# Optimization experiments

Hardware: AMD Instinct MI355X
Metric: run time of the kernel (lower is better)

Reference implementation:

```python
import jax, jax.numpy as jnp
import numpy as np

NI = 2048           # per-node feature dim
H = 2 * NI          # flattened per-sample GRU state (2 nodes)
BS = 4096
NO = 1
NUM_ROUNDS = 2


def setup_inputs() -> dict:
    key = jax.random.key(0)
    ks = jax.random.split(key, 8)
    s_ih = 1.0 / np.sqrt(H)
    features = jax.random.normal(ks[0], (BS, 2, NI), dtype=jnp.float32)
    # torch.nn.GRUCell(H, H): weight_ih [3H, H], weight_hh [3H, H], biases [3H]
    W_ih = jax.random.uniform(ks[1], (3 * H, H), minval=-s_ih, maxval=s_ih, dtype=jnp.float32)
    b_ih = jax.random.uniform(ks[2], (3 * H,), minval=-s_ih, maxval=s_ih, dtype=jnp.float32)
    W_hh = jax.random.uniform(ks[3], (3 * H, H), minval=-s_ih, maxval=s_ih, dtype=jnp.float32)
    b_hh = jax.random.uniform(ks[4], (3 * H,), minval=-s_ih, maxval=s_ih, dtype=jnp.float32)
    # fc = nn.Linear(2*ni, no)
    fc_w = jax.random.uniform(ks[5], (NO, H), minval=-s_ih, maxval=s_ih, dtype=jnp.float32)
    fc_b = jax.random.uniform(ks[6], (NO,), minval=-s_ih, maxval=s_ih, dtype=jnp.float32)
    return {"features": features, "W_ih": W_ih, "b_ih": b_ih,
            "W_hh": W_hh, "b_hh": b_hh, "fc_w": fc_w, "fc_b": fc_b}


def _gru_cell(x, h, W_ih, b_ih, W_hh, b_hh):
    # torch GRUCell semantics
    gi = x @ W_ih.T + b_ih              # [bs, 3H]
    gh = h @ W_hh.T + b_hh              # [bs, 3H]
    i_r, i_z, i_n = jnp.split(gi, 3, axis=-1)
    h_r, h_z, h_n = jnp.split(gh, 3, axis=-1)
    r = jax.nn.sigmoid(i_r + h_r)
    z = jax.nn.sigmoid(i_z + h_z)
    n = jnp.tanh(i_n + r * h_n)
    return (1.0 - z) * n + z * h


def reference(features, W_ih, b_ih, W_hh, b_hh, fc_w, fc_b):
    bs = features.shape[0]
    ni = features.shape[2]
    h = features.reshape(bs, -1)        # [bs, 2*ni] = node0 || node1
    for _ in range(NUM_ROUNDS):
        # fully-connected 2-node graph, sum-aggregate of neighbor messages:
        # node0 receives h1, node1 receives h0 -> x is the half-swap of h
        x = jnp.concatenate([h[:, ni:], h[:, :ni]], axis=-1)
        h = _gru_cell(x, h, W_ih, b_ih, W_hh, b_hh)
    return h @ fc_w.T + fc_b            # [bs, no]
```

## Files before the change

kernel.cpp:

```cpp
#include <hip/hip_runtime.h>


typedef __bf16 bf16x8 __attribute__((ext_vector_type(8)));
typedef float  f32x4  __attribute__((ext_vector_type(4)));
typedef unsigned short u16x4 __attribute__((ext_vector_type(4)));

#define HH    4096
#define NI_D  2048
#define N3H   12288
#define N6H   24576
#define BSZ   4096
#define BM    256
#define BN    256
#define BK    64
#define MT    (BSZ / BM)
#define NT    (N6H / BN)
#define GRID_GEMM (MT * NT)
#define NKT   (HH / BK)

#define NB_W  98304
#define NB_C  16384

__device__ __forceinline__ unsigned short f2bf(float f) {
  unsigned u = __float_as_uint(f);
  u += 0x7FFFu + ((u >> 16) & 1u);
  return (unsigned short)(u >> 16);
}
__device__ __forceinline__ float bf2f(unsigned short s) {
  return __uint_as_float(((unsigned)s) << 16);
}

__device__ __forceinline__ void gload16(const void* g, void* l) {
  void* gv = (void*)g;
  __builtin_amdgcn_global_load_lds(
      (__attribute__((address_space(1))) unsigned int*)gv,
      (__attribute__((address_space(3))) unsigned int*)l,
      16, 0, 0);
}

__global__ void __launch_bounds__(256)
prep(const float* __restrict__ Wih, const float* __restrict__ Whh,
     const float* __restrict__ feat,
     unsigned short* __restrict__ Wc, unsigned short* __restrict__ hb)
{
  int bid = blockIdx.x;
  if (bid < NB_W) {
    int idx = (bid * 256 + threadIdx.x) << 2;
    int j = idx >> 12;
    int k = idx & 4095;
    const float* src;
    if (j < N3H) src = Wih + (size_t)j * HH + ((k + NI_D) & (HH - 1));
    else         src = Whh + (size_t)(j - N3H) * HH + k;
    f32x4 v = *(const f32x4*)src;
    u16x4 o = { f2bf(v[0]), f2bf(v[1]), f2bf(v[2]), f2bf(v[3]) };
    *(u16x4*)(Wc + idx) = o;
  } else {
    int i = ((bid - NB_W) * 256 + threadIdx.x) << 2;
    f32x4 v = *(const f32x4*)(feat + i);
    u16x4 o = { f2bf(v[0]), f2bf(v[1]), f2bf(v[2]), f2bf(v[3]) };
    *(u16x4*)(hb + i) = o;
  }
}

__device__ __forceinline__ void stageA(const char* a_base, char* lds, int ldst,
                                       int d, int kt, int g) {
  int kc = (kt < NKT) ? kt : 0;
  gload16(a_base + (size_t)kc * 128 + (size_t)g * 524288,
          lds + d * 32768 + g * 8192 + ldst);
}
__device__ __forceinline__ void stageB(const char* b_base, char* lds, int ldst,
                                       int d, int kt, int g) {
  int kc = (kt < NKT) ? kt : 0;
  gload16(b_base + (size_t)kc * 128 + (size_t)g * 524288,
          lds + 65536 + d * 32768 + g * 8192 + ldst);
}

template <int MB, int NB>
__device__ __forceinline__ void mfmaQ(f32x4 (&acc)[8][4],
                                      const bf16x8 (&af)[4][2],
                                      const bf16x8 (&bf)[2][2]) {
  __builtin_amdgcn_s_setprio(1);
#pragma unroll
  for (int ks = 0; ks < 2; ++ks)
#pragma unroll
    for (int mf = 0; mf < 4; ++mf)
#pragma unroll
      for (int nf = 0; nf < 2; ++nf)
        acc[MB + mf][NB + nf] = __builtin_amdgcn_mfma_f32_16x16x32_bf16(
            af[mf][ks], bf[nf][ks], acc[MB + mf][NB + nf], 0, 0, 0);
  __builtin_amdgcn_s_setprio(0);
}

#define BAR   __builtin_amdgcn_s_barrier()
#define SB    __builtin_amdgcn_sched_barrier(0)
#define LGKM0 do { asm volatile("s_waitcnt lgkmcnt(0)" ::: "memory"); SB; } while (0)
#define VM6   asm volatile("s_waitcnt vmcnt(6)" ::: "memory")

template <int D>
__device__ __forceinline__ void kblock(char* lds, const char* a_base,
                                       const char* b_base, int ldst,
                                       int aro, int bro, int offk0, int offk1,
                                       int t1, int t2, f32x4 (&acc)[8][4],
                                       bf16x8 (&a47c)[4][2], bf16x8 (&b01c)[2][2],
                                       bf16x8 (&a47n)[4][2], bf16x8 (&b01n)[2][2]) {
  const char* LA  = lds + D * 32768 + aro;
  const char* LB  = lds + 65536 + D * 32768 + bro;
  const char* LAn = lds + (D ^ 1) * 32768 + aro;
  const char* LBn = lds + 65536 + (D ^ 1) * 32768 + bro;
  bf16x8 a03[4][2], b23[2][2];

  LGKM0;
#pragma unroll
  for (int nf = 0; nf < 2; ++nf) {
    b23[nf][0] = *(const bf16x8*)(LB + (2 + nf) * 2048 + offk0);
    b23[nf][1] = *(const bf16x8*)(LB + (2 + nf) * 2048 + offk1);
  }
  stageA(a_base, lds, ldst, D ^ 1, t1, 0);
  stageA(a_base, lds, ldst, D ^ 1, t1, 2);
  SB;
  mfmaQ<4, 0>(acc, a47c, b01c);
  VM6;
  BAR;

  LGKM0;
#pragma unroll
  for (int mf = 0; mf < 4; ++mf) {
    a03[mf][0] = *(const bf16x8*)(LA + mf * 2048 + offk0);
    a03[mf][1] = *(const bf16x8*)(LA + mf * 2048 + offk1);
  }
  stageA(a_base, lds, ldst, D, t2, 1);
  stageA(a_base, lds, ldst, D, t2, 3);
  SB;
  mfmaQ<4, 2>(acc, a47c, b23);
  BAR;

  LGKM0;
  stageB(b_base, lds, ldst, D, t2, 0);
  stageB(b_base, lds, ldst, D, t2, 1);
  SB;
  mfmaQ<0, 0>(acc, a03, b01c);
  VM6;
  BAR;

#pragma unroll
  for (int mf = 0; mf < 4; ++mf) {
    a47n[mf][0] = *(const bf16x8*)(LAn + (4 + mf) * 2048 + offk0);
    a47n[mf][1] = *(const bf16x8*)(LAn + (4 + mf) * 2048 + offk1);
  }
#pragma unroll
  for (int nf = 0; nf < 2; ++nf) {
    b01n[nf][0] = *(const bf16x8*)(LBn + nf * 2048 + offk0);
    b01n[nf][1] = *(const bf16x8*)(LBn + nf * 2048 + offk1);
  }
  stageB(b_base, lds, ldst, D, t2, 2);
  stageB(b_base, lds, ldst, D, t2, 3);
  SB;
  mfmaQ<0, 2>(acc, a03, b23);
  BAR;
}

__global__ void __launch_bounds__(512, 2)
gemm_bt(const unsigned short* __restrict__ A,
        const unsigned short* __restrict__ B,
        unsigned short* __restrict__ C)
{
  __shared__ alignas(16) char lds[131072];

  int bid = blockIdx.x;
  int wg  = (bid & 7) * (GRID_GEMM / 8) + (bid >> 3);
  int nt  = wg / MT;
  int mt  = wg % MT;
  int m0  = mt * BM;
  int n0  = nt * BN;

  int t  = threadIdx.x;
  int wv = t >> 6;
  int l  = t & 63;
  int wm = wv >> 2;
  int wn = wv & 3;

  int rloc   = wv * 8 + (l >> 3);
  int sg_col = ((l & 7) ^ (l >> 3)) << 4;
  const char* a_base = (const char*)A + (size_t)(m0 + rloc) * 8192 + sg_col;
  const char* b_base = (const char*)B + (size_t)(n0 + rloc) * 8192 + sg_col;
  int ldst = wv * 1024;

  int offk0 = ((l >> 4) << 4) ^ ((l & 7) << 4);
  int offk1 = offk0 ^ 64;
  int aro = (wm * 128 + (l & 15)) * 128;
  int bro = (wn * 64  + (l & 15)) * 128;

  f32x4 acc[8][4] = {};
  bf16x8 a47A[4][2], b01A[2][2], a47B[4][2], b01B[2][2];

#pragma unroll
  for (int g = 0; g < 4; ++g) stageA(a_base, lds, ldst, 0, 0, g);
#pragma unroll
  for (int g = 0; g < 4; ++g) stageB(b_base, lds, ldst, 0, 0, g);
  stageA(a_base, lds, ldst, 1, 1, 1);
  stageA(a_base, lds, ldst, 1, 1, 3);
#pragma unroll
  for (int g = 0; g < 4; ++g) stageB(b_base, lds, ldst, 1, 1, g);
  asm volatile("s_waitcnt vmcnt(6)" ::: "memory");
  BAR;
  {
    const char* LA0 = lds + aro;
    const char* LB0 = lds + 65536 + bro;
#pragma unroll
    for (int mf = 0; mf < 4; ++mf) {
      a47A[mf][0] = *(const bf16x8*)(LA0 + (4 + mf) * 2048 + offk0);
      a47A[mf][1] = *(const bf16x8*)(LA0 + (4 + mf) * 2048 + offk1);
    }
#pragma unroll
    for (int nf = 0; nf < 2; ++nf) {
      b01A[nf][0] = *(const bf16x8*)(LB0 + nf * 2048 + offk0);
      b01A[nf][1] = *(const bf16x8*)(LB0 + nf * 2048 + offk1);
    }
  }

#pragma unroll 1
  for (int tt = 0; tt < NKT; tt += 2) {
    kblock<0>(lds, a_base, b_base, ldst, aro, bro, offk0, offk1,
              tt + 1, tt + 2, acc, a47A, b01A, a47B, b01B);
    kblock<1>(lds, a_base, b_base, ldst, aro, bro, offk0, offk1,
              tt + 2, tt + 3, acc, a47B, b01B, a47A, b01A);
  }
  asm volatile("s_waitcnt vmcnt(0) lgkmcnt(0)" ::: "memory");

  int crow = m0 + wm * 128 + ((l >> 4) << 2);
  int ccol = n0 + wn * 64 + (l & 15);
#pragma unroll
  for (int mf = 0; mf < 8; ++mf)
#pragma unroll
    for (int nf = 0; nf < 4; ++nf)
#pragma unroll
      for (int i = 0; i < 4; ++i)
        C[(size_t)(crow + mf * 16 + i) * N6H + (ccol + nf * 16)] =
            f2bf(acc[mf][nf][i]);
}

__global__ void __launch_bounds__(256)
gru1(const unsigned short* __restrict__ C, const float* __restrict__ h_old,
     const float* __restrict__ b_ih, const float* __restrict__ b_hh,
     unsigned short* __restrict__ h_bf)
{
  int idx = blockIdx.x * 256 + threadIdx.x;
  int b = idx >> 10;
  int j = (idx & 1023) << 2;
  const unsigned short* Cr = C + (size_t)b * N6H;
  u16x4 gir = *(const u16x4*)(Cr + j);
  u16x4 giz = *(const u16x4*)(Cr + HH + j);
  u16x4 gin = *(const u16x4*)(Cr + 2 * HH + j);
  u16x4 ghr = *(const u16x4*)(Cr + 3 * HH + j);
  u16x4 ghz = *(const u16x4*)(Cr + 4 * HH + j);
  u16x4 ghn = *(const u16x4*)(Cr + 5 * HH + j);
  f32x4 bir = *(const f32x4*)(b_ih + j);
  f32x4 biz = *(const f32x4*)(b_ih + HH + j);
  f32x4 bin = *(const f32x4*)(b_ih + 2 * HH + j);
  f32x4 bhr = *(const f32x4*)(b_hh + j);
  f32x4 bhz = *(const f32x4*)(b_hh + HH + j);
  f32x4 bhn = *(const f32x4*)(b_hh + 2 * HH + j);
  f32x4 ho  = *(const f32x4*)(h_old + (size_t)b * HH + j);
  u16x4 hb;
#pragma unroll
  for (int e = 0; e < 4; ++e) {
    float r = 1.f / (1.f + expf(-(bf2f(gir[e]) + bir[e] + bf2f(ghr[e]) + bhr[e])));
    float z = 1.f / (1.f + expf(-(bf2f(giz[e]) + biz[e] + bf2f(ghz[e]) + bhz[e])));
    float n = tanhf(bf2f(gin[e]) + bin[e] + r * (bf2f(ghn[e]) + bhn[e]));
    hb[e] = f2bf((1.f - z) * n + z * ho[e]);
  }
  *(u16x4*)(h_bf + (size_t)b * HH + j) = hb;
}

__global__ void __launch_bounds__(256)
gru2_fc(const unsigned short* __restrict__ C,
        const unsigned short* __restrict__ h_old_bf,
        const float* __restrict__ b_ih, const float* __restrict__ b_hh,
        const float* __restrict__ fcw, const float* __restrict__ fcb,
        float* __restrict__ out)
{
  int idx = blockIdx.x * 256 + threadIdx.x;
  int b = idx >> 10;
  int j = (idx & 1023) << 2;
  const unsigned short* Cr = C + (size_t)b * N6H;
  u16x4 gir = *(const u16x4*)(Cr + j);
  u16x4 giz = *(const u16x4*)(Cr + HH + j);
  u16x4 gin = *(const u16x4*)(Cr + 2 * HH + j);
  u16x4 ghr = *(const u16x4*)(Cr + 3 * HH + j);
  u16x4 ghz = *(const u16x4*)(Cr + 4 * HH + j);
  u16x4 ghn = *(const u16x4*)(Cr + 5 * HH + j);
  f32x4 bir = *(const f32x4*)(b_ih + j);
  f32x4 biz = *(const f32x4*)(b_ih + HH + j);
  f32x4 bin = *(const f32x4*)(b_ih + 2 * HH + j);
  f32x4 bhr = *(const f32x4*)(b_hh + j);
  f32x4 bhz = *(const f32x4*)(b_hh + HH + j);
  f32x4 bhn = *(const f32x4*)(b_hh + 2 * HH + j);
  u16x4 hob = *(const u16x4*)(h_old_bf + (size_t)b * HH + j);
  f32x4 fw  = *(const f32x4*)(fcw + j);
  float s = 0.f;
#pragma unroll
  for (int e = 0; e < 4; ++e) {
    float r = 1.f / (1.f + expf(-(bf2f(gir[e]) + bir[e] + bf2f(ghr[e]) + bhr[e])));
    float z = 1.f / (1.f + expf(-(bf2f(giz[e]) + biz[e] + bf2f(ghz[e]) + bhz[e])));
    float n = tanhf(bf2f(gin[e]) + bin[e] + r * (bf2f(ghn[e]) + bhn[e]));
    float h = (1.f - z) * n + z * bf2f(hob[e]);
    s += h * fw[e];
  }
#pragma unroll
  for (int off = 32; off > 0; off >>= 1) s += __shfl_down(s, off);
  __shared__ float red[4];
  if ((threadIdx.x & 63) == 0) red[threadIdx.x >> 6] = s;
  __syncthreads();
  if (threadIdx.x == 0) {
    float v = red[0] + red[1] + red[2] + red[3];
    if ((blockIdx.x & 3) == 0) v += fcb[0];
    atomicAdd(&out[b], v);
  }
}

extern "C" void kernel_launch(void* const* d_in, const int* in_sizes, int n_in,
                              void* d_out, int out_size, void* d_ws, size_t ws_size,
                              hipStream_t stream)
{
  const float* feat = (const float*)d_in[0];
  const float* Wih  = (const float*)d_in[1];
  const float* bih  = (const float*)d_in[2];
  const float* Whh  = (const float*)d_in[3];
  const float* bhh  = (const float*)d_in[4];
  const float* fcw  = (const float*)d_in[5];
  const float* fcb  = (const float*)d_in[6];
  float* out = (float*)d_out;

  char* ws = (char*)d_ws;
  unsigned short* Wc   = (unsigned short*)ws;
  unsigned short* Cbuf = (unsigned short*)(ws + 201326592);
  unsigned short* hb   = (unsigned short*)(ws + 402653184);

  hipMemsetAsync(out, 0, (size_t)out_size * sizeof(float), stream);
  prep<<<NB_W + NB_C, 256, 0, stream>>>(Wih, Whh, feat, Wc, hb);

  gemm_bt<<<GRID_GEMM, 512, 0, stream>>>(hb, Wc, Cbuf);
  gru1<<<16384, 256, 0, stream>>>(Cbuf, feat, bih, bhh, hb);

  gemm_bt<<<GRID_GEMM, 512, 0, stream>>>(hb, Wc, Cbuf);
  gru2_fc<<<16384, 256, 0, stream>>>(Cbuf, hb, bih, bhh, fcw, fcb, out);
}
```

Baseline: 1.503 ms.

## Triple-buffer B tiles in LDS to prefetch weights further ahead

Adds a third LDS buffer for the B (weight) operand so B tiles are loaded three k-steps ahead while A stays double-buffered. The main loop is unrolled by six with rotating buffer indices, a fixed tail, and adjusted vmcnt waits. The intent is to hide more global-load latency behind MFMA work. The cost is larger LDS use, which may limit occupancy, and more code size.

```diff
diff --git a/kernel.cpp b/kernel.cpp
--- a/kernel.cpp
+++ b/kernel.cpp
@@ -69,10 +69,10 @@
           lds + d * 32768 + g * 8192 + ldst);
 }
 __device__ __forceinline__ void stageB(const char* b_base, char* lds, int ldst,
-                                       int d, int kt, int g) {
+                                       int q, int kt, int g) {
   int kc = (kt < NKT) ? kt : 0;
   gload16(b_base + (size_t)kc * 128 + (size_t)g * 524288,
-          lds + 65536 + d * 32768 + g * 8192 + ldst);
+          lds + 65536 + q * 32768 + g * 8192 + ldst);
 }
 
 template <int MB, int NB>
@@ -94,19 +94,21 @@
 #define BAR   __builtin_amdgcn_s_barrier()
 #define SB    __builtin_amdgcn_sched_barrier(0)
 #define LGKM0 do { asm volatile("s_waitcnt lgkmcnt(0)" ::: "memory"); SB; } while (0)
-#define VM6   asm volatile("s_waitcnt vmcnt(6)" ::: "memory")
-
-template <int D>
+#define VM8   asm volatile("s_waitcnt vmcnt(8)" ::: "memory")
+#define VM10  asm volatile("s_waitcnt vmcnt(10)" ::: "memory")
+
+template <int AD, int BD, int BD1>
 __device__ __forceinline__ void kblock(char* lds, const char* a_base,
                                        const char* b_base, int ldst,
                                        int aro, int bro, int offk0, int offk1,
-                                       int t1, int t2, f32x4 (&acc)[8][4],
+                                       int tA1, int tA2, int tB3,
+                                       f32x4 (&acc)[8][4],
                                        bf16x8 (&a47c)[4][2], bf16x8 (&b01c)[2][2],
                                        bf16x8 (&a47n)[4][2], bf16x8 (&b01n)[2][2]) {
-  const char* LA  = lds + D * 32768 + aro;
-  const char* LB  = lds + 65536 + D * 32768 + bro;
-  const char* LAn = lds + (D ^ 1) * 32768 + aro;
-  const char* LBn = lds + 65536 + (D ^ 1) * 32768 + bro;
+  const char* LA  = lds + AD * 32768 + aro;
+  const char* LB  = lds + 65536 + BD * 32768 + bro;
+  const char* LAn = lds + (AD ^ 1) * 32768 + aro;
+  const char* LBn = lds + 65536 + BD1 * 32768 + bro;
   bf16x8 a03[4][2], b23[2][2];
 
   LGKM0;
@@ -115,11 +117,11 @@
     b23[nf][0] = *(const bf16x8*)(LB + (2 + nf) * 2048 + offk0);
     b23[nf][1] = *(const bf16x8*)(LB + (2 + nf) * 2048 + offk1);
   }
-  stageA(a_base, lds, ldst, D ^ 1, t1, 0);
-  stageA(a_base, lds, ldst, D ^ 1, t1, 2);
+  stageA(a_base, lds, ldst, AD ^ 1, tA1, 0);
+  stageA(a_base, lds, ldst, AD ^ 1, tA1, 2);
   SB;
   mfmaQ<4, 0>(acc, a47c, b01c);
-  VM6;
+  VM8;
   BAR;
 
   LGKM0;
@@ -128,18 +130,18 @@
     a03[mf][0] = *(const bf16x8*)(LA + mf * 2048 + offk0);
     a03[mf][1] = *(const bf16x8*)(LA + mf * 2048 + offk1);
   }
-  stageA(a_base, lds, ldst, D, t2, 1);
-  stageA(a_base, lds, ldst, D, t2, 3);
+  stageA(a_base, lds, ldst, AD, tA2, 1);
+  stageA(a_base, lds, ldst, AD, tA2, 3);
   SB;
   mfmaQ<4, 2>(acc, a47c, b23);
   BAR;
 
   LGKM0;
-  stageB(b_base, lds, ldst, D, t2, 0);
-  stageB(b_base, lds, ldst, D, t2, 1);
+  stageB(b_base, lds, ldst, BD, tB3, 0);
+  stageB(b_base, lds, ldst, BD, tB3, 1);
   SB;
   mfmaQ<0, 0>(acc, a03, b01c);
-  VM6;
+  VM10;
   BAR;
 
 #pragma unroll
@@ -152,8 +154,8 @@
     b01n[nf][0] = *(const bf16x8*)(LBn + nf * 2048 + offk0);
     b01n[nf][1] = *(const bf16x8*)(LBn + nf * 2048 + offk1);
   }
-  stageB(b_base, lds, ldst, D, t2, 2);
-  stageB(b_base, lds, ldst, D, t2, 3);
+  stageB(b_base, lds, ldst, BD, tB3, 2);
+  stageB(b_base, lds, ldst, BD, tB3, 3);
   SB;
   mfmaQ<0, 2>(acc, a03, b23);
   BAR;
@@ -164,7 +166,7 @@
         const unsigned short* __restrict__ B,
         unsigned short* __restrict__ C)
 {
-  __shared__ alignas(16) char lds[131072];
+  __shared__ alignas(16) char lds[163840];
 
   int bid = blockIdx.x;
   int wg  = (bid & 7) * (GRID_GEMM / 8) + (bid >> 3);
@@ -194,14 +196,18 @@
   bf16x8 a47A[4][2], b01A[2][2], a47B[4][2], b01B[2][2];
 
 #pragma unroll
-  for (int g = 0; g < 4; ++g) stageA(a_base, lds, ldst, 0, 0, g);
-#pragma unroll
   for (int g = 0; g < 4; ++g) stageB(b_base, lds, ldst, 0, 0, g);
+  stageA(a_base, lds, ldst, 0, 0, 1);
+  stageA(a_base, lds, ldst, 0, 0, 3);
+#pragma unroll
+  for (int g = 0; g < 4; ++g) stageB(b_base, lds, ldst, 1, 1, g);
+  stageA(a_base, lds, ldst, 0, 0, 0);
+  stageA(a_base, lds, ldst, 0, 0, 2);
   stageA(a_base, lds, ldst, 1, 1, 1);
   stageA(a_base, lds, ldst, 1, 1, 3);
 #pragma unroll
-  for (int g = 0; g < 4; ++g) stageB(b_base, lds, ldst, 1, 1, g);
-  asm volatile("s_waitcnt vmcnt(6)" ::: "memory");
+  for (int g = 0; g < 4; ++g) stageB(b_base, lds, ldst, 2, 2, g);
+  asm volatile("s_waitcnt vmcnt(12)" ::: "memory");
   BAR;
   {
     const char* LA0 = lds + aro;
@@ -219,12 +225,28 @@
   }
 
 #pragma unroll 1
-  for (int tt = 0; tt < NKT; tt += 2) {
-    kblock<0>(lds, a_base, b_base, ldst, aro, bro, offk0, offk1,
-              tt + 1, tt + 2, acc, a47A, b01A, a47B, b01B);
-    kblock<1>(lds, a_base, b_base, ldst, aro, bro, offk0, offk1,
-              tt + 2, tt + 3, acc, a47B, b01B, a47A, b01A);
-  }
+  for (int tt = 0; tt < 60; tt += 6) {
+    kblock<0, 0, 1>(lds, a_base, b_base, ldst, aro, bro, offk0, offk1,
+                    tt + 1, tt + 2, tt + 3, acc, a47A, b01A, a47B, b01B);
+    kblock<1, 1, 2>(lds, a_base, b_base, ldst, aro, bro, offk0, offk1,
+                    tt + 2, tt + 3, tt + 4, acc, a47B, b01B, a47A, b01A);
+    kblock<0, 2, 0>(lds, a_base, b_base, ldst, aro, bro, offk0, offk1,
+                    tt + 3, tt + 4, tt + 5, acc, a47A, b01A, a47B, b01B);
+    kblock<1, 0, 1>(lds, a_base, b_base, ldst, aro, bro, offk0, offk1,
+                    tt + 4, tt + 5, tt + 6, acc, a47B, b01B, a47A, b01A);
+    kblock<0, 1, 2>(lds, a_base, b_base, ldst, aro, bro, offk0, offk1,
+                    tt + 5, tt + 6, tt + 7, acc, a47A, b01A, a47B, b01B);
+    kblock<1, 2, 0>(lds, a_base, b_base, ldst, aro, bro, offk0, offk1,
+                    tt + 6, tt + 7, tt + 8, acc, a47B, b01B, a47A, b01A);
+  }
+  kblock<0, 0, 1>(lds, a_base, b_base, ldst, aro, bro, offk0, offk1,
+                  61, 62, 63, acc, a47A, b01A, a47B, b01B);
+  kblock<1, 1, 2>(lds, a_base, b_base, ldst, aro, bro, offk0, offk1,
+                  62, 63, 64, acc, a47B, b01B, a47A, b01A);
+  kblock<0, 2, 0>(lds, a_base, b_base, ldst, aro, bro, offk0, offk1,
+                  63, 64, 65, acc, a47A, b01A, a47B, b01B);
+  kblock<1, 0, 1>(lds, a_base, b_base, ldst, aro, bro, offk0, offk1,
+                  64, 65, 66, acc, a47B, b01B, a47A, b01A);
   asm volatile("s_waitcnt vmcnt(0) lgkmcnt(0)" ::: "memory");
 
   int crow = m0 + wm * 128 + ((l >> 4) << 2);
```

Measured after the change: 1.997 ms. +32.9%, slower.

## Fuse GRU gate epilogue into GEMM via gate-interleaved weight rows

Applied to the files above, without the earlier changes.

The weight rows are reordered so each output tile of 192 columns holds all six gate pre-activations for 32 hidden units. This lets the GRU nonlinearity, and the final FC reduction in round two, run directly in the GEMM epilogue through an LDS staging buffer. The change removes the large bf16 gate-buffer write and re-read and the two separate elementwise GRU kernels. In exchange the N tile shrinks from 256 to 192, which changes MFMA per LDS-load balance and the grid size, and adds an epilogue phase with scalar LDS and global reads.

```diff
diff --git a/kernel.cpp b/kernel.cpp
--- a/kernel.cpp
+++ b/kernel.cpp
@@ -4,6 +4,7 @@
 typedef __bf16 bf16x8 __attribute__((ext_vector_type(8)));
 typedef float  f32x4  __attribute__((ext_vector_type(4)));
 typedef unsigned short u16x4 __attribute__((ext_vector_type(4)));
+typedef unsigned short u16x8 __attribute__((ext_vector_type(8)));
 
 #define HH    4096
 #define NI_D  2048
@@ -11,11 +12,11 @@
 #define N6H   24576
 #define BSZ   4096
 #define BM    256
-#define BN    256
+#define BN    192
 #define BK    64
 #define MT    (BSZ / BM)
-#define NT    (N6H / BN)
-#define GRID_GEMM (MT * NT)
+#define NTN   (N6H / BN)
+#define GRID_GEMM (MT * NTN)
 #define NKT   (HH / BK)
 
 #define NB_W  98304
@@ -41,16 +42,18 @@
 __global__ void __launch_bounds__(256)
 prep(const float* __restrict__ Wih, const float* __restrict__ Whh,
      const float* __restrict__ feat,
-     unsigned short* __restrict__ Wc, unsigned short* __restrict__ hb)
+     unsigned short* __restrict__ Wc, unsigned short* __restrict__ hb0)
 {
   int bid = blockIdx.x;
   if (bid < NB_W) {
     int idx = (bid * 256 + threadIdx.x) << 2;
-    int j = idx >> 12;
+    int r = idx >> 12;
     int k = idx & 4095;
+    int jg = r / 6;
+    int g  = r - jg * 6;
     const float* src;
-    if (j < N3H) src = Wih + (size_t)j * HH + ((k + NI_D) & (HH - 1));
-    else         src = Whh + (size_t)(j - N3H) * HH + k;
+    if (g < 3) src = Wih + ((size_t)g * HH + jg) * HH + ((k + NI_D) & (HH - 1));
+    else       src = Whh + ((size_t)(g - 3) * HH + jg) * HH + k;
     f32x4 v = *(const f32x4*)src;
     u16x4 o = { f2bf(v[0]), f2bf(v[1]), f2bf(v[2]), f2bf(v[3]) };
     *(u16x4*)(Wc + idx) = o;
@@ -58,7 +61,7 @@
     int i = ((bid - NB_W) * 256 + threadIdx.x) << 2;
     f32x4 v = *(const f32x4*)(feat + i);
     u16x4 o = { f2bf(v[0]), f2bf(v[1]), f2bf(v[2]), f2bf(v[3]) };
-    *(u16x4*)(hb + i) = o;
+    *(u16x4*)(hb0 + i) = o;
   }
 }
 
@@ -72,22 +75,35 @@
                                        int d, int kt, int g) {
   int kc = (kt < NKT) ? kt : 0;
   gload16(b_base + (size_t)kc * 128 + (size_t)g * 524288,
-          lds + 65536 + d * 32768 + g * 8192 + ldst);
-}
-
-template <int MB, int NB>
-__device__ __forceinline__ void mfmaQ(f32x4 (&acc)[8][4],
+          lds + 65536 + d * 24576 + g * 8192 + ldst);
+}
+
+template <int MB>
+__device__ __forceinline__ void mfmaQ16(f32x4 (&acc)[8][3],
+                                        const bf16x8 (&af)[4][2],
+                                        const bf16x8 (&bf)[2][2]) {
+  __builtin_amdgcn_s_setprio(1);
+#pragma unroll
+  for (int ks = 0; ks < 2; ++ks)
+#pragma unroll
+    for (int mf = 0; mf < 4; ++mf)
+#pragma unroll
+      for (int nf = 0; nf < 2; ++nf)
+        acc[MB + mf][nf] = __builtin_amdgcn_mfma_f32_16x16x32_bf16(
+            af[mf][ks], bf[nf][ks], acc[MB + mf][nf], 0, 0, 0);
+  __builtin_amdgcn_s_setprio(0);
+}
+template <int MB>
+__device__ __forceinline__ void mfma8(f32x4 (&acc)[8][3],
                                       const bf16x8 (&af)[4][2],
-                                      const bf16x8 (&bf)[2][2]) {
+                                      const bf16x8 (&b2)[2]) {
   __builtin_amdgcn_s_setprio(1);
 #pragma unroll
   for (int ks = 0; ks < 2; ++ks)
 #pragma unroll
     for (int mf = 0; mf < 4; ++mf)
-#pragma unroll
-      for (int nf = 0; nf < 2; ++nf)
-        acc[MB + mf][NB + nf] = __builtin_amdgcn_mfma_f32_16x16x32_bf16(
-            af[mf][ks], bf[nf][ks], acc[MB + mf][NB + nf], 0, 0, 0);
+      acc[MB + mf][2] = __builtin_amdgcn_mfma_f32_16x16x32_bf16(
+          af[mf][ks], b2[ks], acc[MB + mf][2], 0, 0, 0);
   __builtin_amdgcn_s_setprio(0);
 }
 
@@ -100,25 +116,22 @@
 __device__ __forceinline__ void kblock(char* lds, const char* a_base,
                                        const char* b_base, int ldst,
                                        int aro, int bro, int offk0, int offk1,
-                                       int t1, int t2, f32x4 (&acc)[8][4],
+                                       int t1, int t2, f32x4 (&acc)[8][3],
                                        bf16x8 (&a47c)[4][2], bf16x8 (&b01c)[2][2],
                                        bf16x8 (&a47n)[4][2], bf16x8 (&b01n)[2][2]) {
   const char* LA  = lds + D * 32768 + aro;
-  const char* LB  = lds + 65536 + D * 32768 + bro;
+  const char* LB  = lds + 65536 + D * 24576 + bro;
   const char* LAn = lds + (D ^ 1) * 32768 + aro;
-  const char* LBn = lds + 65536 + (D ^ 1) * 32768 + bro;
-  bf16x8 a03[4][2], b23[2][2];
+  const char* LBn = lds + 65536 + (D ^ 1) * 24576 + bro;
+  bf16x8 a03[4][2], b2[2];
 
   LGKM0;
-#pragma unroll
-  for (int nf = 0; nf < 2; ++nf) {
-    b23[nf][0] = *(const bf16x8*)(LB + (2 + nf) * 2048 + offk0);
-    b23[nf][1] = *(const bf16x8*)(LB + (2 + nf) * 2048 + offk1);
-  }
+  b2[0] = *(const bf16x8*)(LB + 2 * 2048 + offk0);
+  b2[1] = *(const bf16x8*)(LB + 2 * 2048 + offk1);
   stageA(a_base, lds, ldst, D ^ 1, t1, 0);
   stageA(a_base, lds, ldst, D ^ 1, t1, 2);
   SB;
-  mfmaQ<4, 0>(acc, a47c, b01c);
+  mfmaQ16<4>(acc, a47c, b01c);
   VM6;
   BAR;
 
@@ -131,14 +144,14 @@
   stageA(a_base, lds, ldst, D, t2, 1);
   stageA(a_base, lds, ldst, D, t2, 3);
   SB;
-  mfmaQ<4, 2>(acc, a47c, b23);
+  mfma8<4>(acc, a47c, b2);
   BAR;
 
   LGKM0;
   stageB(b_base, lds, ldst, D, t2, 0);
   stageB(b_base, lds, ldst, D, t2, 1);
   SB;
-  mfmaQ<0, 0>(acc, a03, b01c);
+  mfmaQ16<0>(acc, a03, b01c);
   VM6;
   BAR;
 
@@ -153,18 +166,23 @@
     b01n[nf][1] = *(const bf16x8*)(LBn + nf * 2048 + offk1);
   }
   stageB(b_base, lds, ldst, D, t2, 2);
-  stageB(b_base, lds, ldst, D, t2, 3);
   SB;
-  mfmaQ<0, 2>(acc, a03, b23);
-  BAR;
-}
-
+  mfma8<0>(acc, a03, b2);
+  BAR;
+}
+
+template <bool R2>
 __global__ void __launch_bounds__(512, 2)
-gemm_bt(const unsigned short* __restrict__ A,
-        const unsigned short* __restrict__ B,
-        unsigned short* __restrict__ C)
+gemm_gru(const unsigned short* __restrict__ A,
+         const unsigned short* __restrict__ B,
+         const float* __restrict__ hold_f32,
+         const unsigned short* __restrict__ hold_bf,
+         const float* __restrict__ b_ih, const float* __restrict__ b_hh,
+         unsigned short* __restrict__ h_out,
+         const float* __restrict__ fcw, const float* __restrict__ fcb,
+         float* __restrict__ out)
 {
-  __shared__ alignas(16) char lds[131072];
+  __shared__ alignas(16) char lds[114688];
 
   int bid = blockIdx.x;
   int wg  = (bid & 7) * (GRID_GEMM / 8) + (bid >> 3);
@@ -173,9 +191,9 @@
   int m0  = mt * BM;
   int n0  = nt * BN;
 
-  int t  = threadIdx.x;
-  int wv = t >> 6;
-  int l  = t & 63;
+  int tix = threadIdx.x;
+  int wv = tix >> 6;
+  int l  = tix & 63;
   int wm = wv >> 2;
   int wn = wv & 3;
 
@@ -188,20 +206,24 @@
   int offk0 = ((l >> 4) << 4) ^ ((l & 7) << 4);
   int offk1 = offk0 ^ 64;
   int aro = (wm * 128 + (l & 15)) * 128;
-  int bro = (wn * 64  + (l & 15)) * 128;
-
-  f32x4 acc[8][4] = {};
+  int bro = (wn * 48  + (l & 15)) * 128;
+
+  f32x4 acc[8][3] = {};
   bf16x8 a47A[4][2], b01A[2][2], a47B[4][2], b01B[2][2];
 
-#pragma unroll
-  for (int g = 0; g < 4; ++g) stageA(a_base, lds, ldst, 0, 0, g);
-#pragma unroll
-  for (int g = 0; g < 4; ++g) stageB(b_base, lds, ldst, 0, 0, g);
+  stageB(b_base, lds, ldst, 0, 0, 0);
+  stageB(b_base, lds, ldst, 0, 0, 1);
+  stageB(b_base, lds, ldst, 0, 0, 2);
+  stageA(a_base, lds, ldst, 0, 0, 1);
+  stageA(a_base, lds, ldst, 0, 0, 3);
+  stageA(a_base, lds, ldst, 0, 0, 0);
+  stageA(a_base, lds, ldst, 0, 0, 2);
   stageA(a_base, lds, ldst, 1, 1, 1);
   stageA(a_base, lds, ldst, 1, 1, 3);
-#pragma unroll
-  for (int g = 0; g < 4; ++g) stageB(b_base, lds, ldst, 1, 1, g);
-  asm volatile("s_waitcnt vmcnt(6)" ::: "memory");
+  stageB(b_base, lds, ldst, 1, 1, 0);
+  stageB(b_base, lds, ldst, 1, 1, 1);
+  stageB(b_base, lds, ldst, 1, 1, 2);
+  asm volatile("s_waitcnt vmcnt(7)" ::: "memory");
   BAR;
   {
     const char* LA0 = lds + aro;
@@ -226,95 +248,67 @@
               tt + 2, tt + 3, acc, a47B, b01B, a47A, b01A);
   }
   asm volatile("s_waitcnt vmcnt(0) lgkmcnt(0)" ::: "memory");
-
-  int crow = m0 + wm * 128 + ((l >> 4) << 2);
-  int ccol = n0 + wn * 64 + (l & 15);
-#pragma unroll
-  for (int mf = 0; mf < 8; ++mf)
-#pragma unroll
-    for (int nf = 0; nf < 4; ++nf)
-#pragma unroll
-      for (int i = 0; i < 4; ++i)
-        C[(size_t)(crow + mf * 16 + i) * N6H + (ccol + nf * 16)] =
-            f2bf(acc[mf][nf][i]);
-}
-
-__global__ void __launch_bounds__(256)
-gru1(const unsigned short* __restrict__ C, const float* __restrict__ h_old,
-     const float* __restrict__ b_ih, const float* __restrict__ b_hh,
-     unsigned short* __restrict__ h_bf)
-{
-  int idx = blockIdx.x * 256 + threadIdx.x;
-  int b = idx >> 10;
-  int j = (idx & 1023) << 2;
-  const unsigned short* Cr = C + (size_t)b * N6H;
-  u16x4 gir = *(const u16x4*)(Cr + j);
-  u16x4 giz = *(const u16x4*)(Cr + HH + j);
-  u16x4 gin = *(const u16x4*)(Cr + 2 * HH + j);
-  u16x4 ghr = *(const u16x4*)(Cr + 3 * HH + j);
-  u16x4 ghz = *(const u16x4*)(Cr + 4 * HH + j);
-  u16x4 ghn = *(const u16x4*)(Cr + 5 * HH + j);
-  f32x4 bir = *(const f32x4*)(b_ih + j);
-  f32x4 biz = *(const f32x4*)(b_ih + HH + j);
-  f32x4 bin = *(const f32x4*)(b_ih + 2 * HH + j);
-  f32x4 bhr = *(const f32x4*)(b_hh + j);
-  f32x4 bhz = *(const f32x4*)(b_hh + HH + j);
-  f32x4 bhn = *(const f32x4*)(b_hh + 2 * HH + j);
-  f32x4 ho  = *(const f32x4*)(h_old + (size_t)b * HH + j);
-  u16x4 hb;
-#pragma unroll
-  for (int e = 0; e < 4; ++e) {
-    float r = 1.f / (1.f + expf(-(bf2f(gir[e]) + bir[e] + bf2f(ghr[e]) + bhr[e])));
-    float z = 1.f / (1.f + expf(-(bf2f(giz[e]) + biz[e] + bf2f(ghz[e]) + bhz[e])));
-    float n = tanhf(bf2f(gin[e]) + bin[e] + r * (bf2f(ghn[e]) + bhn[e]));
-    hb[e] = f2bf((1.f - z) * n + z * ho[e]);
-  }
-  *(u16x4*)(h_bf + (size_t)b * HH + j) = hb;
-}
-
-__global__ void __launch_bounds__(256)
-gru2_fc(const unsigned short* __restrict__ C,
-        const unsigned short* __restrict__ h_old_bf,
-        const float* __restrict__ b_ih, const float* __restrict__ b_hh,
-        const float* __restrict__ fcw, const float* __restrict__ fcb,
-        float* __restrict__ out)
-{
-  int idx = blockIdx.x * 256 + threadIdx.x;
-  int b = idx >> 10;
-  int j = (idx & 1023) << 2;
-  const unsigned short* Cr = C + (size_t)b * N6H;
-  u16x4 gir = *(const u16x4*)(Cr + j);
-  u16x4 giz = *(const u16x4*)(Cr + HH + j);
-  u16x4 gin = *(const u16x4*)(Cr + 2 * HH + j);
-  u16x4 ghr = *(const u16x4*)(Cr + 3 * HH + j);
-  u16x4 ghz = *(const u16x4*)(Cr + 4 * HH + j);
-  u16x4 ghn = *(const u16x4*)(Cr + 5 * HH + j);
-  f32x4 bir = *(const f32x4*)(b_ih + j);
-  f32x4 biz = *(const f32x4*)(b_ih + HH + j);
-  f32x4 bin = *(const f32x4*)(b_ih + 2 * HH + j);
-  f32x4 bhr = *(const f32x4*)(b_hh + j);
-  f32x4 bhz = *(const f32x4*)(b_hh + HH + j);
-  f32x4 bhn = *(const f32x4*)(b_hh + 2 * HH + j);
-  u16x4 hob = *(const u16x4*)(h_old_bf + (size_t)b * HH + j);
-  f32x4 fw  = *(const f32x4*)(fcw + j);
-  float s = 0.f;
-#pragma unroll
-  for (int e = 0; e < 4; ++e) {
-    float r = 1.f / (1.f + expf(-(bf2f(gir[e]) + bir[e] + bf2f(ghr[e]) + bhr[e])));
-    float z = 1.f / (1.f + expf(-(bf2f(giz[e]) + biz[e] + bf2f(ghz[e]) + bhz[e])));
-    float n = tanhf(bf2f(gin[e]) + bin[e] + r * (bf2f(ghn[e]) + bhn[e]));
-    float h = (1.f - z) * n + z * bf2f(hob[e]);
-    s += h * fw[e];
-  }
-#pragma unroll
-  for (int off = 32; off > 0; off >>= 1) s += __shfl_down(s, off);
-  __shared__ float red[4];
-  if ((threadIdx.x & 63) == 0) red[threadIdx.x >> 6] = s;
-  __syncthreads();
-  if (threadIdx.x == 0) {
-    float v = red[0] + red[1] + red[2] + red[3];
-    if ((blockIdx.x & 3) == 0) v += fcb[0];
-    atomicAdd(&out[b], v);
+  BAR;
+
+  {
+    int crow0 = wm * 128 + ((l >> 4) << 2);
+    int ccol  = wn * 48 + (l & 15);
+#pragma unroll
+    for (int mf = 0; mf < 8; ++mf)
+#pragma unroll
+      for (int nf = 0; nf < 3; ++nf)
+#pragma unroll
+        for (int i = 0; i < 4; ++i)
+          *(unsigned short*)(lds + (crow0 + mf * 16 + i) * 392 +
+                             (ccol + nf * 16) * 2) = f2bf(acc[mf][nf][i]);
+  }
+  BAR;
+
+  {
+    int b   = tix >> 1;
+    int bg  = m0 + b;
+    int jlb = (tix & 1) << 4;
+    const char* Lrow = lds + b * 392;
+    float s = 0.f;
+    u16x8 h0 = {}, h1 = {};
+#pragma unroll
+    for (int jj = 0; jj < 16; ++jj) {
+      int jl = jlb + jj;
+      int jg = nt * 32 + jl;
+      unsigned g01 = *(const unsigned*)(Lrow + jl * 12);
+      unsigned g23 = *(const unsigned*)(Lrow + jl * 12 + 4);
+      unsigned g45 = *(const unsigned*)(Lrow + jl * 12 + 8);
+      float gir = bf2f((unsigned short)(g01 & 0xffff));
+      float giz = bf2f((unsigned short)(g01 >> 16));
+      float gin = bf2f((unsigned short)(g23 & 0xffff));
+      float ghr = bf2f((unsigned short)(g23 >> 16));
+      float ghz = bf2f((unsigned short)(g45 & 0xffff));
+      float ghn = bf2f((unsigned short)(g45 >> 16));
+      float ho;
+      if constexpr (R2) ho = bf2f(hold_bf[(size_t)bg * HH + jg]);
+      else              ho = hold_f32[(size_t)bg * HH + jg];
+      float r = 1.f / (1.f + expf(-(gir + b_ih[jg] + ghr + b_hh[jg])));
+      float z = 1.f / (1.f + expf(-(giz + b_ih[HH + jg] + ghz + b_hh[HH + jg])));
+      float n = tanhf(gin + b_ih[2 * HH + jg] + r * (ghn + b_hh[2 * HH + jg]));
+      float h = (1.f - z) * n + z * ho;
+      if constexpr (R2) {
+        s += h * fcw[jg];
+      } else {
+        unsigned short hv = f2bf(h);
+        if (jj < 8) h0[jj] = hv; else h1[jj - 8] = hv;
+      }
+    }
+    if constexpr (R2) {
+      s += __shfl_down(s, 1);
+      if ((tix & 1) == 0) {
+        if (nt == 0) s += fcb[0];
+        atomicAdd(&out[bg], s);
+      }
+    } else {
+      unsigned short* hp = h_out + (size_t)bg * HH + nt * 32 + jlb;
+      *(u16x8*)hp = h0;
+      *(u16x8*)(hp + 8) = h1;
+    }
   }
 }
 
@@ -332,16 +326,15 @@
   float* out = (float*)d_out;
 
   char* ws = (char*)d_ws;
-  unsigned short* Wc   = (unsigned short*)ws;
-  unsigned short* Cbuf = (unsigned short*)(ws + 201326592);
-  unsigned short* hb   = (unsigned short*)(ws + 402653184);
+  unsigned short* Wc  = (unsigned short*)ws;
+  unsigned short* hb0 = (unsigned short*)(ws + 201326592);
+  unsigned short* hb1 = (unsigned short*)(ws + 234881024);
 
   hipMemsetAsync(out, 0, (size_t)out_size * sizeof(float), stream);
-  prep<<<NB_W + NB_C, 256, 0, stream>>>(Wih, Whh, feat, Wc, hb);
-
-  gemm_bt<<<GRID_GEMM, 512, 0, stream>>>(hb, Wc, Cbuf);
-  gru1<<<16384, 256, 0, stream>>>(Cbuf, feat, bih, bhh, hb);
-
-  gemm_bt<<<GRID_GEMM, 512, 0, stream>>>(hb, Wc, Cbuf);
-  gru2_fc<<<16384, 256, 0, stream>>>(Cbuf, hb, bih, bhh, fcw, fcb, out);
-}
+  prep<<<NB_W + NB_C, 256, 0, stream>>>(Wih, Whh, feat, Wc, hb0);
+
+  gemm_gru<false><<<GRID_GEMM, 512, 0, stream>>>(
+      hb0, Wc, feat, nullptr, bih, bhh, hb1, fcw, fcb, out);
+  gemm_gru<true><<<GRID_GEMM, 512, 0, stream>>>(
+      hb1, Wc, nullptr, hb1, bih, bhh, nullptr, fcw, fcb, out);
+}
```

After: 1.577 ms. 4.9% more time.

## Restructure GEMM k-loop into two half phases with full B-fragment register prefetch

Applied to the files above, without the earlier changes.

Reorganizes the GEMM main loop from four quarter-tile MFMA phases per k-block into two half-tile phases. All four B fragments are now prefetched into registers, and the B-tile global stages move to the start of the block. The aim is to cut barriers and LDS wait points per k-step and to give longer uninterrupted MFMA runs. The cost is more live VGPRs for the extra B fragments, which could cause register spills or lower occupancy at 2 blocks/CU. The revised vmcnt accounting and LDS buffer reuse also carry a correctness risk.

```diff
diff --git a/kernel.cpp b/kernel.cpp
--- a/kernel.cpp
+++ b/kernel.cpp
@@ -75,73 +75,67 @@
           lds + 65536 + d * 32768 + g * 8192 + ldst);
 }
 
-template <int MB, int NB>
-__device__ __forceinline__ void mfmaQ(f32x4 (&acc)[8][4],
+template <int MB>
+__device__ __forceinline__ void mfmaH(f32x4 (&acc)[8][4],
                                       const bf16x8 (&af)[4][2],
-                                      const bf16x8 (&bf)[2][2]) {
+                                      const bf16x8 (&b01)[2][2],
+                                      const bf16x8 (&b23)[2][2]) {
   __builtin_amdgcn_s_setprio(1);
 #pragma unroll
   for (int ks = 0; ks < 2; ++ks)
 #pragma unroll
-    for (int mf = 0; mf < 4; ++mf)
-#pragma unroll
-      for (int nf = 0; nf < 2; ++nf)
-        acc[MB + mf][NB + nf] = __builtin_amdgcn_mfma_f32_16x16x32_bf16(
-            af[mf][ks], bf[nf][ks], acc[MB + mf][NB + nf], 0, 0, 0);
+    for (int mf = 0; mf < 4; ++mf) {
+      acc[MB + mf][0] = __builtin_amdgcn_mfma_f32_16x16x32_bf16(
+          af[mf][ks], b01[0][ks], acc[MB + mf][0], 0, 0, 0);
+      acc[MB + mf][1] = __builtin_amdgcn_mfma_f32_16x16x32_bf16(
+          af[mf][ks], b01[1][ks], acc[MB + mf][1], 0, 0, 0);
+      acc[MB + mf][2] = __builtin_amdgcn_mfma_f32_16x16x32_bf16(
+          af[mf][ks], b23[0][ks], acc[MB + mf][2], 0, 0, 0);
+      acc[MB + mf][3] = __builtin_amdgcn_mfma_f32_16x16x32_bf16(
+          af[mf][ks], b23[1][ks], acc[MB + mf][3], 0, 0, 0);
+    }
   __builtin_amdgcn_s_setprio(0);
 }
 
 #define BAR   __builtin_amdgcn_s_barrier()
 #define SB    __builtin_amdgcn_sched_barrier(0)
 #define LGKM0 do { asm volatile("s_waitcnt lgkmcnt(0)" ::: "memory"); SB; } while (0)
-#define VM6   asm volatile("s_waitcnt vmcnt(6)" ::: "memory")
+#define VM2   asm volatile("s_waitcnt vmcnt(2)" ::: "memory")
 
 template <int D>
 __device__ __forceinline__ void kblock(char* lds, const char* a_base,
                                        const char* b_base, int ldst,
                                        int aro, int bro, int offk0, int offk1,
                                        int t1, int t2, f32x4 (&acc)[8][4],
-                                       bf16x8 (&a47c)[4][2], bf16x8 (&b01c)[2][2],
-                                       bf16x8 (&a47n)[4][2], bf16x8 (&b01n)[2][2]) {
+                                       bf16x8 (&a47c)[4][2],
+                                       bf16x8 (&b01c)[2][2], bf16x8 (&b23c)[2][2],
+                                       bf16x8 (&a47n)[4][2],
+                                       bf16x8 (&b01n)[2][2], bf16x8 (&b23n)[2][2]) {
   const char* LA  = lds + D * 32768 + aro;
-  const char* LB  = lds + 65536 + D * 32768 + bro;
   const char* LAn = lds + (D ^ 1) * 32768 + aro;
   const char* LBn = lds + 65536 + (D ^ 1) * 32768 + bro;
-  bf16x8 a03[4][2], b23[2][2];
+  bf16x8 a03[4][2];
 
   LGKM0;
-#pragma unroll
-  for (int nf = 0; nf < 2; ++nf) {
-    b23[nf][0] = *(const bf16x8*)(LB + (2 + nf) * 2048 + offk0);
-    b23[nf][1] = *(const bf16x8*)(LB + (2 + nf) * 2048 + offk1);
-  }
   stageA(a_base, lds, ldst, D ^ 1, t1, 0);
   stageA(a_base, lds, ldst, D ^ 1, t1, 2);
-  SB;
-  mfmaQ<4, 0>(acc, a47c, b01c);
-  VM6;
-  BAR;
-
-  LGKM0;
+  stageB(b_base, lds, ldst, D ^ 1, t1, 0);
+  stageB(b_base, lds, ldst, D ^ 1, t1, 1);
+  stageB(b_base, lds, ldst, D ^ 1, t1, 2);
+  stageB(b_base, lds, ldst, D ^ 1, t1, 3);
 #pragma unroll
   for (int mf = 0; mf < 4; ++mf) {
     a03[mf][0] = *(const bf16x8*)(LA + mf * 2048 + offk0);
     a03[mf][1] = *(const bf16x8*)(LA + mf * 2048 + offk1);
   }
+  SB;
+  mfmaH<4>(acc, a47c, b01c, b23c);
+  BAR;
+
   stageA(a_base, lds, ldst, D, t2, 1);
   stageA(a_base, lds, ldst, D, t2, 3);
-  SB;
-  mfmaQ<4, 2>(acc, a47c, b23);
-  BAR;
-
+  VM2;
   LGKM0;
-  stageB(b_base, lds, ldst, D, t2, 0);
-  stageB(b_base, lds, ldst, D, t2, 1);
-  SB;
-  mfmaQ<0, 0>(acc, a03, b01c);
-  VM6;
-  BAR;
-
 #pragma unroll
   for (int mf = 0; mf < 4; ++mf) {
     a47n[mf][0] = *(const bf16x8*)(LAn + (4 + mf) * 2048 + offk0);
@@ -151,11 +145,11 @@
   for (int nf = 0; nf < 2; ++nf) {
     b01n[nf][0] = *(const bf16x8*)(LBn + nf * 2048 + offk0);
     b01n[nf][1] = *(const bf16x8*)(LBn + nf * 2048 + offk1);
-  }
-  stageB(b_base, lds, ldst, D, t2, 2);
-  stageB(b_base, lds, ldst, D, t2, 3);
+    b23n[nf][0] = *(const bf16x8*)(LBn + (2 + nf) * 2048 + offk0);
+    b23n[nf][1] = *(const bf16x8*)(LBn + (2 + nf) * 2048 + offk1);
+  }
   SB;
-  mfmaQ<0, 2>(acc, a03, b23);
+  mfmaH<0>(acc, a03, b01c, b23c);
   BAR;
 }
 
@@ -191,17 +185,18 @@
   int bro = (wn * 64  + (l & 15)) * 128;
 
   f32x4 acc[8][4] = {};
-  bf16x8 a47A[4][2], b01A[2][2], a47B[4][2], b01B[2][2];
-
-#pragma unroll
-  for (int g = 0; g < 4; ++g) stageA(a_base, lds, ldst, 0, 0, g);
+  bf16x8 a47A[4][2], b01A[2][2], b23A[2][2];
+  bf16x8 a47B[4][2], b01B[2][2], b23B[2][2];
+
+  stageA(a_base, lds, ldst, 0, 0, 1);
+  stageA(a_base, lds, ldst, 0, 0, 3);
+  stageA(a_base, lds, ldst, 0, 0, 0);
+  stageA(a_base, lds, ldst, 0, 0, 2);
 #pragma unroll
   for (int g = 0; g < 4; ++g) stageB(b_base, lds, ldst, 0, 0, g);
   stageA(a_base, lds, ldst, 1, 1, 1);
   stageA(a_base, lds, ldst, 1, 1, 3);
-#pragma unroll
-  for (int g = 0; g < 4; ++g) stageB(b_base, lds, ldst, 1, 1, g);
-  asm volatile("s_waitcnt vmcnt(6)" ::: "memory");
+  asm volatile("s_waitcnt vmcnt(2)" ::: "memory");
   BAR;
   {
     const char* LA0 = lds + aro;
@@ -215,15 +210,17 @@
     for (int nf = 0; nf < 2; ++nf) {
       b01A[nf][0] = *(const bf16x8*)(LB0 + nf * 2048 + offk0);
       b01A[nf][1] = *(const bf16x8*)(LB0 + nf * 2048 + offk1);
+      b23A[nf][0] = *(const bf16x8*)(LB0 + (2 + nf) * 2048 + offk0);
+      b23A[nf][1] = *(const bf16x8*)(LB0 + (2 + nf) * 2048 + offk1);
     }
   }
 
 #pragma unroll 1
   for (int tt = 0; tt < NKT; tt += 2) {
     kblock<0>(lds, a_base, b_base, ldst, aro, bro, offk0, offk1,
-              tt + 1, tt + 2, acc, a47A, b01A, a47B, b01B);
+              tt + 1, tt + 2, acc, a47A, b01A, b23A, a47B, b01B, b23B);
     kblock<1>(lds, a_base, b_base, ldst, aro, bro, offk0, offk1,
-              tt + 2, tt + 3, acc, a47B, b01B, a47A, b01A);
+              tt + 2, tt + 3, acc, a47B, b01B, b23B, a47A, b01A, b23A);
   }
   asm volatile("s_waitcnt vmcnt(0) lgkmcnt(0)" ::: "memory");
 
```

After: 2.674 ms. 1.78x slower.
